# Performance work log

Hardware: AMD Instinct MI355X
Metric: run time of the kernel (lower is better)

## Reference

```python
import jax, jax.numpy as jnp
import numpy as np

NUM_HEADS = 8
NEG_INF = float(-2**32 + 1)
LN_EPS = 1e-8


def setup_inputs() -> dict:
    key = jax.random.key(0)
    ks = jax.random.split(key, 9)
    B, T, D = 4, 2048, 512
    inp = {
        "queries": jax.random.normal(ks[0], (B, T, D), jnp.float32),
        "keys": jax.random.normal(ks[1], (B, T, D), jnp.float32),
        "values": jax.random.normal(ks[2], (B, T, D), jnp.float32),
        "Wq": jax.random.normal(ks[3], (D, D), jnp.float32) / np.sqrt(D),
        "bq": jnp.zeros((D,), jnp.float32),
        "Wk": jax.random.normal(ks[4], (D, D), jnp.float32) / np.sqrt(D),
        "bk": jnp.zeros((D,), jnp.float32),
        "Wv": jax.random.normal(ks[5], (D, D), jnp.float32) / np.sqrt(D),
        "bv": jnp.zeros((D,), jnp.float32),
        "gamma": jnp.ones((D,), jnp.float32),
        "beta": jnp.zeros((D,), jnp.float32),
    }
    return inp


def _split_heads(x, h):
    # torch.cat(torch.chunk(x, h, dim=2), dim=0): [B,T,D] -> [h*B, T, D/h], head-major
    B, T, D = x.shape
    return x.reshape(B, T, h, D // h).transpose(2, 0, 1, 3).reshape(h * B, T, D // h)


def _merge_heads(x, h, B):
    # inverse: [h*B, T, dh] -> [B, T, h*dh]
    hB, T, dh = x.shape
    return x.reshape(h, B, T, dh).transpose(1, 2, 0, 3).reshape(B, T, h * dh)


def reference(queries, keys, values, Wq, bq, Wk, bk, Wv, bv, gamma, beta):
    h = NUM_HEADS
    B, Tq, D = queries.shape
    dh = D // h

    Q = jax.nn.relu(queries @ Wq + bq)
    K = jax.nn.relu(keys @ Wk + bk)
    V = jax.nn.relu(values @ Wv + bv)

    Q_ = _split_heads(Q, h)  # [h*B, Tq, dh]
    K_ = _split_heads(K, h)
    V_ = _split_heads(V, h)

    scores = jnp.einsum('bqd,bkd->bqk', Q_, K_) / jnp.sqrt(jnp.float32(dh))  # [h*B, Tq, Tk]

    # key padding mask: zero rows in `keys` get -inf scores
    key_mask = jnp.sign(jnp.abs(jnp.sum(keys, axis=-1)))  # [B, Tk]
    key_mask = jnp.tile(key_mask, (h, 1))  # [h*B, Tk]
    scores = jnp.where(key_mask[:, None, :] == 0.0, NEG_INF, scores)

    attn = jax.nn.softmax(scores, axis=-1)

    # query mask applied multiplicatively post-softmax
    query_mask = jnp.sign(jnp.abs(jnp.sum(queries, axis=-1)))  # [B, Tq]
    query_mask = jnp.tile(query_mask, (h, 1))  # [h*B, Tq]
    attn = attn * query_mask[:, :, None]

    out = jnp.einsum('bqk,bkd->bqd', attn, V_)  # [h*B, Tq, dh]
    out = _merge_heads(out, h, B) + queries  # residual

    # custom LayerNorm: torch.std is unbiased (ddof=1), eps added to std
    mean = out.mean(-1, keepdims=True)
    std = jnp.sqrt(out.var(-1, ddof=1, keepdims=True))
    return gamma * (out - mean) / (std + LN_EPS) + beta
```

## Files before the change

kernel.cpp:

```cpp
#include <hip/hip_runtime.h>


typedef __attribute__((ext_vector_type(8))) __bf16 bf16x8;
typedef __attribute__((ext_vector_type(4))) float f32x4;

#if __has_builtin(__builtin_amdgcn_exp2f)
#define EXP2F __builtin_amdgcn_exp2f
#else
#define EXP2F exp2f
#endif

#define QSCALE (0.125f * 1.4426950408889634f)

__device__ __forceinline__ unsigned short f2bf(float f) {
  return __builtin_bit_cast(unsigned short, (__bf16)f);
}
__device__ __forceinline__ unsigned pk2(float a, float b) {
  return (unsigned)f2bf(a) | ((unsigned)f2bf(b) << 16);
}
__device__ __forceinline__ f32x4 mfma16(bf16x8 a, bf16x8 b, f32x4 c) {
  return __builtin_amdgcn_mfma_f32_16x16x32_bf16(a, b, c, 0, 0, 0);
}
__device__ __forceinline__ bf16x8 ld_bf8(const unsigned short* p) {
  return *(const bf16x8*)p;
}
__device__ __forceinline__ void g2l16(const void* g, void* l) {
  __builtin_amdgcn_global_load_lds(
      (const __attribute__((address_space(1))) void*)g,
      (__attribute__((address_space(3))) void*)l, 16, 0, 0);
}

__global__ __launch_bounds__(256) void wt_kernel(const float* __restrict__ Wq,
                                                 const float* __restrict__ Wk,
                                                 const float* __restrict__ Wv,
                                                 unsigned short* __restrict__ Wt) {
  int idx = blockIdx.x * 256 + threadIdx.x;
  int o = idx * 8;
  int z = o >> 18;
  int rem = o & 262143;
  int n = rem >> 9;
  int k0 = rem & 511;
  const float* W = (z == 0) ? Wq : ((z == 1) ? Wk : Wv);
  unsigned int w[4];
#pragma unroll
  for (int i = 0; i < 4; ++i) {
    unsigned short lo = f2bf(W[(k0 + 2 * i) * 512 + n]);
    unsigned short hi = f2bf(W[(k0 + 2 * i + 1) * 512 + n]);
    w[i] = (unsigned)lo | ((unsigned)hi << 16);
  }
  *(uint4*)(Wt + o) = make_uint4(w[0], w[1], w[2], w[3]);
}

__global__ __launch_bounds__(256, 3) void proj_kernel(
    const float* __restrict__ Xq, const float* __restrict__ Xk,
    const float* __restrict__ Xv, const float* __restrict__ bq,
    const float* __restrict__ bk, const float* __restrict__ bv,
    const unsigned short* __restrict__ Wt, unsigned short* __restrict__ Qb,
    unsigned short* __restrict__ Kb, unsigned short* __restrict__ Vt,
    float* __restrict__ qmask, float* __restrict__ kmask) {
  __shared__ float Asm[2][128][16];
  __shared__ unsigned short Bsm[128][32];

  int tid = threadIdx.x;
  int m0g = blockIdx.x * 128;
  int z = m0g >> 13;
  int m0 = m0g & 8191;
  int n0 = blockIdx.y * 128;
  const float* X = (z == 0) ? Xq : ((z == 1) ? Xk : Xv);
  const float* bias = (z == 0) ? bq : ((z == 1) ? bk : bv);
  const unsigned short* Wz = Wt + z * 262144;

  int w = tid >> 6, lane = tid & 63;
  int wm = w >> 1, wn = w & 1;
  int mrow = lane & 15, quad = lane >> 4;

  int srow = tid >> 2, schk = tid & 3;
  const float* gA = X + (m0 + srow) * 512 + schk * 4;
  const unsigned short* gB = Wz + (n0 + srow) * 512 + schk * 8;
  char* lA = (char*)&Asm[0][0][0] + tid * 16;
  char* lB = (char*)&Bsm[0][0] + tid * 16;

  const float* rA = &Asm[quad >> 1][0][(quad & 1) * 8];
  const unsigned short* rB = &Bsm[0][quad * 8];

  f32x4 zero = {0.f, 0.f, 0.f, 0.f};
  f32x4 acc[4][4];
#pragma unroll
  for (int i = 0; i < 4; ++i)
#pragma unroll
    for (int j = 0; j < 4; ++j) acc[i][j] = zero;

  bool domask = (z < 2) && (n0 == 0) && (wn == 0);
  float rsum[4] = {0.f, 0.f, 0.f, 0.f};

  for (int kc = 0; kc < 16; ++kc) {
    int ko = kc * 32;
    g2l16(gA + ko, lA);
    g2l16(gA + ko + 64 * 512, lA + 4096);
    g2l16(gA + ko + 16, lA + 8192);
    g2l16(gA + ko + 16 + 64 * 512, lA + 12288);
    g2l16(gB + ko, lB);
    g2l16(gB + ko + 64 * 512, lB + 4096);
    __syncthreads();

    bf16x8 af[4], bfr[4];
#pragma unroll
    for (int mt = 0; mt < 4; ++mt) {
      const float* pa = rA + (wm * 64 + mt * 16 + mrow) * 16;
      f32x4 lo = *(const f32x4*)pa;
      f32x4 hi = *(const f32x4*)(pa + 4);
      if (domask)
        rsum[mt] += lo[0] + lo[1] + lo[2] + lo[3] + hi[0] + hi[1] + hi[2] + hi[3];
      bf16x8 t;
      t[0] = (__bf16)lo[0]; t[1] = (__bf16)lo[1];
      t[2] = (__bf16)lo[2]; t[3] = (__bf16)lo[3];
      t[4] = (__bf16)hi[0]; t[5] = (__bf16)hi[1];
      t[6] = (__bf16)hi[2]; t[7] = (__bf16)hi[3];
      af[mt] = t;
    }
#pragma unroll
    for (int nt = 0; nt < 4; ++nt)
      bfr[nt] = ld_bf8(rB + (wn * 64 + nt * 16 + mrow) * 32);
#pragma unroll
    for (int mt = 0; mt < 4; ++mt)
#pragma unroll
      for (int nt = 0; nt < 4; ++nt)
        acc[mt][nt] = mfma16(af[mt], bfr[nt], acc[mt][nt]);
    __syncthreads();
  }

  if (domask) {
    float* msk = (z == 0) ? qmask : kmask;
#pragma unroll
    for (int mt = 0; mt < 4; ++mt) {
      float s = rsum[mt];
      s += __shfl_xor(s, 16);
      s += __shfl_xor(s, 32);
      if (quad == 0)
        msk[m0 + wm * 64 + mt * 16 + mrow] = (s == 0.f) ? 0.f : 1.f;
    }
  }

  if (z < 2) {
    unsigned short* dst = (z == 0) ? Qb : Kb;
    float sc = (z == 0) ? QSCALE : 1.0f;
#pragma unroll
    for (int nt = 0; nt < 4; ++nt) {
      int n = n0 + wn * 64 + nt * 16 + mrow;
      float bv_ = bias[n];
#pragma unroll
      for (int mt = 0; mt < 4; ++mt) {
        int m = m0 + wm * 64 + mt * 16 + quad * 4;
#pragma unroll
        for (int r = 0; r < 4; ++r) {
          float v = fmaxf(acc[mt][nt][r] + bv_, 0.f) * sc;
          dst[(m + r) * 512 + n] = f2bf(v);
        }
      }
    }
  } else {
#pragma unroll
    for (int nt = 0; nt < 4; ++nt) {
      int n = n0 + wn * 64 + nt * 16 + mrow;
      int hh = n >> 6, jj = n & 63;
      float bv_ = bias[n];
#pragma unroll
      for (int mt = 0; mt < 4; ++mt) {
        int grow = m0 + wm * 64 + mt * 16 + quad * 4;
        int bb = grow >> 11, tl = grow & 2047;
        int pos = (tl & ~31) + quad * 8 + (mt & 1) * 4;
        float p0 = fmaxf(acc[mt][nt][0] + bv_, 0.f);
        float p1 = fmaxf(acc[mt][nt][1] + bv_, 0.f);
        float p2 = fmaxf(acc[mt][nt][2] + bv_, 0.f);
        float p3 = fmaxf(acc[mt][nt][3] + bv_, 0.f);
        *(uint2*)(Vt + ((hh * 4 + bb) * 64 + jj) * 2048 + pos) =
            make_uint2(pk2(p0, p1), pk2(p2, p3));
      }
    }
  }
}

__global__ __launch_bounds__(256, 2) void attn_kernel(
    const unsigned short* __restrict__ Qb, const unsigned short* __restrict__ Kb,
    const unsigned short* __restrict__ Vt, const float* __restrict__ qmask,
    const float* __restrict__ kmask, const float* __restrict__ queries,
    float* __restrict__ out) {
  __shared__ char smem[66560];
  unsigned short* KsmS = (unsigned short*)smem;
  unsigned short* VsmS = (unsigned short*)(smem + 32768);
  float* Obuf = (float*)smem;
  float* lbuf = (float*)(smem + 65536);

  int hb = blockIdx.x;
  int qt = blockIdx.y;
  int h = hb >> 2, b = hb & 3;
  int q0 = qt * 128;
  int tid = threadIdx.x;
  int w = tid >> 6, lane = tid & 63;
  int qh = w >> 1, kh2 = w & 1;
  int mrow = lane & 15, quad = lane >> 4;

  const unsigned short* gK =
      Kb + (b * 2048 + (tid >> 3)) * 512 + h * 64 + (((tid & 7) ^ ((tid >> 3) & 7)) * 8);
  const unsigned short* gV =
      Vt + (hb * 64 + (tid >> 4)) * 2048 + (((tid & 15) ^ ((tid >> 4) & 15)) * 8);

  bf16x8 qf[4][2];
  {
    const unsigned short* qp =
        Qb + (b * 2048 + q0 + qh * 64 + mrow) * 512 + h * 64 + quad * 8;
#pragma unroll
    for (int qn = 0; qn < 4; ++qn) {
      qf[qn][0] = ld_bf8(qp + qn * 8192);
      qf[qn][1] = ld_bf8(qp + qn * 8192 + 32);
    }
  }

  f32x4 zero = {0.f, 0.f, 0.f, 0.f};
  f32x4 oacc[4][4];
#pragma unroll
  for (int i = 0; i < 4; ++i)
#pragma unroll
    for (int j = 0; j < 4; ++j) oacc[i][j] = zero;
  float lpart[4] = {0.f, 0.f, 0.f, 0.f};

  const float* kmB = kmask + b * 2048 + kh2 * 64 + quad * 4;
  const int kfrow = kh2 * 64;
  const int mlow = mrow & 7;

#pragma unroll
  for (int j = 0; j < 4; ++j) {
    g2l16(gK + j * 32 * 512, &KsmS[j * 2048 + tid * 8]);
    g2l16(gV + j * 16 * 2048, &VsmS[j * 2048 + tid * 8]);
  }

  for (int it = 0; it < 16; ++it) {
    int bi = it & 1;
    int kb = it * 128;
    __syncthreads();

    if (it < 15) {
      int nkb = kb + 128;
      int nb = 1 - bi;
#pragma unroll
      for (int j = 0; j < 4; ++j) {
        g2l16(gK + (nkb + j * 32) * 512, &KsmS[nb * 8192 + j * 2048 + tid * 8]);
        g2l16(gV + nkb + j * 16 * 2048, &VsmS[nb * 8192 + j * 2048 + tid * 8]);
      }
    }

    f32x4 kmv[4];
#pragma unroll
    for (int mt = 0; mt < 4; ++mt)
      kmv[mt] = *(const f32x4*)(kmB + kb + mt * 16);

#pragma unroll
    for (int kg = 0; kg < 2; ++kg) {
      bf16x8 kfA0 = ld_bf8(&KsmS[bi * 8192 + (kfrow + kg * 32 + mrow) * 64 +
                                 ((quad) ^ mlow) * 8]);
      bf16x8 kfA1 = ld_bf8(&KsmS[bi * 8192 + (kfrow + kg * 32 + mrow) * 64 +
                                 ((4 + quad) ^ mlow) * 8]);
      bf16x8 kfB0 = ld_bf8(&KsmS[bi * 8192 + (kfrow + kg * 32 + 16 + mrow) * 64 +
                                 ((quad) ^ mlow) * 8]);
      bf16x8 kfB1 = ld_bf8(&KsmS[bi * 8192 + (kfrow + kg * 32 + 16 + mrow) * 64 +
                                 ((4 + quad) ^ mlow) * 8]);
      bf16x8 vfg[4];
#pragma unroll
      for (int dt = 0; dt < 4; ++dt)
        vfg[dt] = ld_bf8(&VsmS[bi * 8192 + (dt * 16 + mrow) * 128 +
                               ((kh2 * 8 + kg * 4 + quad) ^ mrow) * 8]);

      f32x4 sA[4], sB[4];
#pragma unroll
      for (int qn = 0; qn < 4; ++qn) {
        f32x4 s0 = mfma16(kfA0, qf[qn][0], zero);
        sA[qn] = mfma16(kfA1, qf[qn][1], s0);
        f32x4 s1 = mfma16(kfB0, qf[qn][0], zero);
        sB[qn] = mfma16(kfB1, qf[qn][1], s1);
      }
#pragma unroll
      for (int qn = 0; qn < 4; ++qn) {
        f32x4 p0, p1;
#pragma unroll
        for (int r = 0; r < 4; ++r) {
          p0[r] = EXP2F(sA[qn][r]) * kmv[kg * 2][r];
          p1[r] = EXP2F(sB[qn][r]) * kmv[kg * 2 + 1][r];
        }
        lpart[qn] += p0[0] + p0[1] + p0[2] + p0[3] + p1[0] + p1[1] + p1[2] + p1[3];
        bf16x8 pf = __builtin_bit_cast(
            bf16x8, make_uint4(pk2(p0[0], p0[1]), pk2(p0[2], p0[3]),
                               pk2(p1[0], p1[1]), pk2(p1[2], p1[3])));
#pragma unroll
        for (int dt = 0; dt < 4; ++dt)
          oacc[dt][qn] = mfma16(pf, vfg[dt], oacc[dt][qn]);
      }
    }
  }

#pragma unroll
  for (int qn = 0; qn < 4; ++qn) {
    lpart[qn] += __shfl_xor(lpart[qn], 16);
    lpart[qn] += __shfl_xor(lpart[qn], 32);
  }
  __syncthreads();
  if (quad == 0) {
#pragma unroll
    for (int qn = 0; qn < 4; ++qn)
      lbuf[kh2 * 128 + qh * 64 + qn * 16 + mrow] = lpart[qn];
  }
  if (kh2 == 1) {
#pragma unroll
    for (int dt = 0; dt < 4; ++dt)
#pragma unroll
      for (int qn = 0; qn < 4; ++qn)
#pragma unroll
        for (int r = 0; r < 4; ++r)
          Obuf[(qh * 64 + qn * 16 + quad * 4 + r) * 65 + dt * 16 + mrow] =
              oacc[dt][qn][r];
  }
  __syncthreads();
  if (kh2 == 0) {
#pragma unroll
    for (int qn = 0; qn < 4; ++qn) {
#pragma unroll
      for (int r = 0; r < 4; ++r) {
        int qrow = qh * 64 + qn * 16 + quad * 4 + r;
        float l = lbuf[qrow] + lbuf[128 + qrow];
        int qg = b * 2048 + q0 + qrow;
        float inv = qmask[qg] / l;
#pragma unroll
        for (int dt = 0; dt < 4; ++dt) {
          int idx = qg * 512 + h * 64 + dt * 16 + mrow;
          out[idx] =
              (oacc[dt][qn][r] + Obuf[qrow * 65 + dt * 16 + mrow]) * inv +
              queries[idx];
        }
      }
    }
  }
}

__global__ __launch_bounds__(256) void ln_kernel(float* __restrict__ out,
                                                 const float* __restrict__ gamma,
                                                 const float* __restrict__ beta) {
  int row = blockIdx.x * 4 + (threadIdx.x >> 6);
  int lane = threadIdx.x & 63;
  float* p = out + row * 512;
  float4 v1 = ((const float4*)p)[lane];
  float4 v2 = ((const float4*)p)[64 + lane];
  float s = v1.x + v1.y + v1.z + v1.w + v2.x + v2.y + v2.z + v2.w;
  float sq = v1.x * v1.x + v1.y * v1.y + v1.z * v1.z + v1.w * v1.w +
             v2.x * v2.x + v2.y * v2.y + v2.z * v2.z + v2.w * v2.w;
#pragma unroll
  for (int off = 32; off > 0; off >>= 1) {
    s += __shfl_xor(s, off);
    sq += __shfl_xor(sq, off);
  }
  float mean = s * (1.f / 512.f);
  float var = fmaxf((sq - 512.f * mean * mean) * (1.f / 511.f), 0.f);
  float inv = 1.f / (sqrtf(var) + 1e-8f);
  float4 g1 = ((const float4*)gamma)[lane];
  float4 g2 = ((const float4*)gamma)[64 + lane];
  float4 b1 = ((const float4*)beta)[lane];
  float4 b2 = ((const float4*)beta)[64 + lane];
  v1.x = g1.x * (v1.x - mean) * inv + b1.x;
  v1.y = g1.y * (v1.y - mean) * inv + b1.y;
  v1.z = g1.z * (v1.z - mean) * inv + b1.z;
  v1.w = g1.w * (v1.w - mean) * inv + b1.w;
  v2.x = g2.x * (v2.x - mean) * inv + b2.x;
  v2.y = g2.y * (v2.y - mean) * inv + b2.y;
  v2.z = g2.z * (v2.z - mean) * inv + b2.z;
  v2.w = g2.w * (v2.w - mean) * inv + b2.w;
  ((float4*)p)[lane] = v1;
  ((float4*)p)[64 + lane] = v2;
}

extern "C" void kernel_launch(void* const* d_in, const int* in_sizes, int n_in,
                              void* d_out, int out_size, void* d_ws, size_t ws_size,
                              hipStream_t stream) {
  (void)in_sizes; (void)n_in; (void)out_size; (void)ws_size;
  const float* queries = (const float*)d_in[0];
  const float* keys    = (const float*)d_in[1];
  const float* values  = (const float*)d_in[2];
  const float* Wq = (const float*)d_in[3];
  const float* bq = (const float*)d_in[4];
  const float* Wk = (const float*)d_in[5];
  const float* bk = (const float*)d_in[6];
  const float* Wv = (const float*)d_in[7];
  const float* bv = (const float*)d_in[8];
  const float* gamma = (const float*)d_in[9];
  const float* beta  = (const float*)d_in[10];
  float* out = (float*)d_out;

  char* ws = (char*)d_ws;
  unsigned short* Qb = (unsigned short*)(ws);
  unsigned short* Kb = (unsigned short*)(ws + 8 * 1024 * 1024);
  unsigned short* Vt = (unsigned short*)(ws + 16 * 1024 * 1024);
  unsigned short* Wt = (unsigned short*)(ws + 24 * 1024 * 1024);
  float* qmask = (float*)(ws + 24 * 1024 * 1024 + 3 * 512 * 512 * 2);
  float* kmask = qmask + 8192;

  wt_kernel<<<384, 256, 0, stream>>>(Wq, Wk, Wv, Wt);
  proj_kernel<<<dim3(192, 4), 256, 0, stream>>>(queries, keys, values, bq, bk, bv,
                                                Wt, Qb, Kb, Vt, qmask, kmask);
  attn_kernel<<<dim3(32, 16), 256, 0, stream>>>(Qb, Kb, Vt, qmask, kmask, queries, out);
  ln_kernel<<<2048, 256, 0, stream>>>(out, gamma, beta);
}
```

Baseline: 190.5 us.

## Split attention over key halves, fuse combine into LayerNorm, double-buffer projection loads

The attention kernel now splits the key range into two halves across a third grid dimension. Each block handles 128 queries with 4 waves of 32 queries and writes unnormalized partial outputs plus row sums, with the row sums computed by an MFMA against a ones vector. The LayerNorm kernel combines the two partials, applies the query mask, normalization and residual, which removes the in-block shared-memory reduction and raises occupancy and grid size. The projection GEMM also double-buffers its shared-memory tiles, dropping one barrier per step. The cost is extra global traffic for the partial output buffer and row sums.

```diff
diff --git a/kernel.cpp b/kernel.cpp
--- a/kernel.cpp
+++ b/kernel.cpp
@@ -58,8 +58,8 @@
     const unsigned short* __restrict__ Wt, unsigned short* __restrict__ Qb,
     unsigned short* __restrict__ Kb, unsigned short* __restrict__ Vt,
     float* __restrict__ qmask, float* __restrict__ kmask) {
-  __shared__ float Asm[2][128][16];
-  __shared__ unsigned short Bsm[128][32];
+  __shared__ float Asm[2][2][128][16];
+  __shared__ unsigned short Bsm[2][128][32];
 
   int tid = threadIdx.x;
   int m0g = blockIdx.x * 128;
@@ -77,11 +77,6 @@
   int srow = tid >> 2, schk = tid & 3;
   const float* gA = X + (m0 + srow) * 512 + schk * 4;
   const unsigned short* gB = Wz + (n0 + srow) * 512 + schk * 8;
-  char* lA = (char*)&Asm[0][0][0] + tid * 16;
-  char* lB = (char*)&Bsm[0][0] + tid * 16;
-
-  const float* rA = &Asm[quad >> 1][0][(quad & 1) * 8];
-  const unsigned short* rB = &Bsm[0][quad * 8];
 
   f32x4 zero = {0.f, 0.f, 0.f, 0.f};
   f32x4 acc[4][4];
@@ -93,15 +88,35 @@
   bool domask = (z < 2) && (n0 == 0) && (wn == 0);
   float rsum[4] = {0.f, 0.f, 0.f, 0.f};
 
+  {
+    char* lA = (char*)&Asm[0][0][0][0] + tid * 16;
+    char* lB = (char*)&Bsm[0][0][0] + tid * 16;
+    g2l16(gA, lA);
+    g2l16(gA + 64 * 512, lA + 4096);
+    g2l16(gA + 16, lA + 8192);
+    g2l16(gA + 16 + 64 * 512, lA + 12288);
+    g2l16(gB, lB);
+    g2l16(gB + 64 * 512, lB + 4096);
+  }
+
   for (int kc = 0; kc < 16; ++kc) {
-    int ko = kc * 32;
-    g2l16(gA + ko, lA);
-    g2l16(gA + ko + 64 * 512, lA + 4096);
-    g2l16(gA + ko + 16, lA + 8192);
-    g2l16(gA + ko + 16 + 64 * 512, lA + 12288);
-    g2l16(gB + ko, lB);
-    g2l16(gB + ko + 64 * 512, lB + 4096);
+    int bi = kc & 1;
     __syncthreads();
+    if (kc < 15) {
+      int ko = (kc + 1) * 32;
+      int nb = 1 - bi;
+      char* lA = (char*)&Asm[nb][0][0][0] + tid * 16;
+      char* lB = (char*)&Bsm[nb][0][0] + tid * 16;
+      g2l16(gA + ko, lA);
+      g2l16(gA + ko + 64 * 512, lA + 4096);
+      g2l16(gA + ko + 16, lA + 8192);
+      g2l16(gA + ko + 16 + 64 * 512, lA + 12288);
+      g2l16(gB + ko, lB);
+      g2l16(gB + ko + 64 * 512, lB + 4096);
+    }
+
+    const float* rA = &Asm[bi][quad >> 1][0][(quad & 1) * 8];
+    const unsigned short* rB = &Bsm[bi][0][quad * 8];
 
     bf16x8 af[4], bfr[4];
 #pragma unroll
@@ -126,7 +141,6 @@
 #pragma unroll
       for (int nt = 0; nt < 4; ++nt)
         acc[mt][nt] = mfma16(af[mt], bfr[nt], acc[mt][nt]);
-    __syncthreads();
   }
 
   if (domask) {
@@ -180,174 +194,164 @@
   }
 }
 
-__global__ __launch_bounds__(256, 2) void attn_kernel(
+__global__ __launch_bounds__(256, 3) void attn_kernel(
     const unsigned short* __restrict__ Qb, const unsigned short* __restrict__ Kb,
-    const unsigned short* __restrict__ Vt, const float* __restrict__ qmask,
-    const float* __restrict__ kmask, const float* __restrict__ queries,
-    float* __restrict__ out) {
-  __shared__ char smem[66560];
-  unsigned short* KsmS = (unsigned short*)smem;
-  unsigned short* VsmS = (unsigned short*)(smem + 32768);
-  float* Obuf = (float*)smem;
-  float* lbuf = (float*)(smem + 65536);
+    const unsigned short* __restrict__ Vt, const float* __restrict__ kmask,
+    float* __restrict__ Out0, float* __restrict__ Out1,
+    float* __restrict__ lsum) {
+  __shared__ unsigned short Ksm[2][4096];
+  __shared__ unsigned short Vsm[2][4096];
 
   int hb = blockIdx.x;
   int qt = blockIdx.y;
+  int ks = blockIdx.z;
   int h = hb >> 2, b = hb & 3;
   int q0 = qt * 128;
+  int k0 = ks * 1024;
   int tid = threadIdx.x;
   int w = tid >> 6, lane = tid & 63;
-  int qh = w >> 1, kh2 = w & 1;
   int mrow = lane & 15, quad = lane >> 4;
-
-  const unsigned short* gK =
-      Kb + (b * 2048 + (tid >> 3)) * 512 + h * 64 + (((tid & 7) ^ ((tid >> 3) & 7)) * 8);
-  const unsigned short* gV =
-      Vt + (hb * 64 + (tid >> 4)) * 2048 + (((tid & 15) ^ ((tid >> 4) & 15)) * 8);
-
-  bf16x8 qf[4][2];
+  int mlow = mrow & 7;
+
+  int srow = tid >> 3;
+  int sslot = (tid & 7) ^ (srow & 7);
+  const unsigned short* gK = Kb + (b * 2048 + k0 + srow) * 512 + h * 64 + sslot * 8;
+  const unsigned short* gV = Vt + (hb * 64 + srow) * 2048 + k0 + sslot * 8;
+
+  bf16x8 qf[2][2];
   {
     const unsigned short* qp =
-        Qb + (b * 2048 + q0 + qh * 64 + mrow) * 512 + h * 64 + quad * 8;
-#pragma unroll
-    for (int qn = 0; qn < 4; ++qn) {
+        Qb + (b * 2048 + q0 + w * 32 + mrow) * 512 + h * 64 + quad * 8;
+#pragma unroll
+    for (int qn = 0; qn < 2; ++qn) {
       qf[qn][0] = ld_bf8(qp + qn * 8192);
       qf[qn][1] = ld_bf8(qp + qn * 8192 + 32);
     }
   }
 
   f32x4 zero = {0.f, 0.f, 0.f, 0.f};
-  f32x4 oacc[4][4];
-#pragma unroll
-  for (int i = 0; i < 4; ++i)
-#pragma unroll
-    for (int j = 0; j < 4; ++j) oacc[i][j] = zero;
-  float lpart[4] = {0.f, 0.f, 0.f, 0.f};
-
-  const float* kmB = kmask + b * 2048 + kh2 * 64 + quad * 4;
-  const int kfrow = kh2 * 64;
-  const int mlow = mrow & 7;
-
-#pragma unroll
-  for (int j = 0; j < 4; ++j) {
-    g2l16(gK + j * 32 * 512, &KsmS[j * 2048 + tid * 8]);
-    g2l16(gV + j * 16 * 2048, &VsmS[j * 2048 + tid * 8]);
-  }
+  f32x4 oacc[4][2];
+#pragma unroll
+  for (int i = 0; i < 4; ++i) {
+    oacc[i][0] = zero;
+    oacc[i][1] = zero;
+  }
+  f32x4 lacc[2] = {zero, zero};
+  bf16x8 ones;
+#pragma unroll
+  for (int i = 0; i < 8; ++i) ones[i] = (__bf16)1.0f;
+
+  g2l16(gK, &Ksm[0][tid * 8]);
+  g2l16(gK + 32 * 512, &Ksm[0][2048 + tid * 8]);
+  g2l16(gV, &Vsm[0][tid * 8]);
+  g2l16(gV + 32 * 2048, &Vsm[0][2048 + tid * 8]);
 
   for (int it = 0; it < 16; ++it) {
     int bi = it & 1;
-    int kb = it * 128;
     __syncthreads();
-
     if (it < 15) {
-      int nkb = kb + 128;
+      int nof = (it + 1) * 64;
       int nb = 1 - bi;
-#pragma unroll
-      for (int j = 0; j < 4; ++j) {
-        g2l16(gK + (nkb + j * 32) * 512, &KsmS[nb * 8192 + j * 2048 + tid * 8]);
-        g2l16(gV + nkb + j * 16 * 2048, &VsmS[nb * 8192 + j * 2048 + tid * 8]);
-      }
-    }
-
-    f32x4 kmv[4];
-#pragma unroll
-    for (int mt = 0; mt < 4; ++mt)
-      kmv[mt] = *(const f32x4*)(kmB + kb + mt * 16);
+      g2l16(gK + nof * 512, &Ksm[nb][tid * 8]);
+      g2l16(gK + (nof + 32) * 512, &Ksm[nb][2048 + tid * 8]);
+      g2l16(gV + nof, &Vsm[nb][tid * 8]);
+      g2l16(gV + nof + 32 * 2048, &Vsm[nb][2048 + tid * 8]);
+    }
+
+    const float* kmc = kmask + b * 2048 + k0 + it * 64 + quad * 4;
+    f32x4 km00 = *(const f32x4*)(kmc);
+    f32x4 km01 = *(const f32x4*)(kmc + 16);
+    f32x4 km10 = *(const f32x4*)(kmc + 32);
+    f32x4 km11 = *(const f32x4*)(kmc + 48);
 
 #pragma unroll
     for (int kg = 0; kg < 2; ++kg) {
-      bf16x8 kfA0 = ld_bf8(&KsmS[bi * 8192 + (kfrow + kg * 32 + mrow) * 64 +
-                                 ((quad) ^ mlow) * 8]);
-      bf16x8 kfA1 = ld_bf8(&KsmS[bi * 8192 + (kfrow + kg * 32 + mrow) * 64 +
-                                 ((4 + quad) ^ mlow) * 8]);
-      bf16x8 kfB0 = ld_bf8(&KsmS[bi * 8192 + (kfrow + kg * 32 + 16 + mrow) * 64 +
-                                 ((quad) ^ mlow) * 8]);
-      bf16x8 kfB1 = ld_bf8(&KsmS[bi * 8192 + (kfrow + kg * 32 + 16 + mrow) * 64 +
-                                 ((4 + quad) ^ mlow) * 8]);
-      bf16x8 vfg[4];
+      bf16x8 kf00 = ld_bf8(&Ksm[bi][(kg * 32 + mrow) * 64 + ((quad) ^ mlow) * 8]);
+      bf16x8 kf01 = ld_bf8(&Ksm[bi][(kg * 32 + mrow) * 64 + ((4 + quad) ^ mlow) * 8]);
+      bf16x8 kf10 = ld_bf8(&Ksm[bi][(kg * 32 + 16 + mrow) * 64 + ((quad) ^ mlow) * 8]);
+      bf16x8 kf11 = ld_bf8(&Ksm[bi][(kg * 32 + 16 + mrow) * 64 + ((4 + quad) ^ mlow) * 8]);
+      bf16x8 vf[4];
 #pragma unroll
       for (int dt = 0; dt < 4; ++dt)
-        vfg[dt] = ld_bf8(&VsmS[bi * 8192 + (dt * 16 + mrow) * 128 +
-                               ((kh2 * 8 + kg * 4 + quad) ^ mrow) * 8]);
-
-      f32x4 sA[4], sB[4];
-#pragma unroll
-      for (int qn = 0; qn < 4; ++qn) {
-        f32x4 s0 = mfma16(kfA0, qf[qn][0], zero);
-        sA[qn] = mfma16(kfA1, qf[qn][1], s0);
-        f32x4 s1 = mfma16(kfB0, qf[qn][0], zero);
-        sB[qn] = mfma16(kfB1, qf[qn][1], s1);
-      }
-#pragma unroll
-      for (int qn = 0; qn < 4; ++qn) {
+        vf[dt] = ld_bf8(&Vsm[bi][(dt * 16 + mrow) * 64 + ((kg * 4 + quad) ^ mlow) * 8]);
+      f32x4 kma = kg ? km10 : km00;
+      f32x4 kmb = kg ? km11 : km01;
+
+#pragma unroll
+      for (int qn = 0; qn < 2; ++qn) {
+        f32x4 s0 = mfma16(kf00, qf[qn][0], zero);
+        s0 = mfma16(kf01, qf[qn][1], s0);
+        f32x4 s1 = mfma16(kf10, qf[qn][0], zero);
+        s1 = mfma16(kf11, qf[qn][1], s1);
         f32x4 p0, p1;
 #pragma unroll
         for (int r = 0; r < 4; ++r) {
-          p0[r] = EXP2F(sA[qn][r]) * kmv[kg * 2][r];
-          p1[r] = EXP2F(sB[qn][r]) * kmv[kg * 2 + 1][r];
+          p0[r] = EXP2F(s0[r]) * kma[r];
+          p1[r] = EXP2F(s1[r]) * kmb[r];
         }
-        lpart[qn] += p0[0] + p0[1] + p0[2] + p0[3] + p1[0] + p1[1] + p1[2] + p1[3];
         bf16x8 pf = __builtin_bit_cast(
             bf16x8, make_uint4(pk2(p0[0], p0[1]), pk2(p0[2], p0[3]),
                                pk2(p1[0], p1[1]), pk2(p1[2], p1[3])));
+        lacc[qn] = mfma16(pf, ones, lacc[qn]);
 #pragma unroll
         for (int dt = 0; dt < 4; ++dt)
-          oacc[dt][qn] = mfma16(pf, vfg[dt], oacc[dt][qn]);
+          oacc[dt][qn] = mfma16(pf, vf[dt], oacc[dt][qn]);
       }
     }
   }
 
-#pragma unroll
-  for (int qn = 0; qn < 4; ++qn) {
-    lpart[qn] += __shfl_xor(lpart[qn], 16);
-    lpart[qn] += __shfl_xor(lpart[qn], 32);
-  }
-  __syncthreads();
-  if (quad == 0) {
-#pragma unroll
-    for (int qn = 0; qn < 4; ++qn)
-      lbuf[kh2 * 128 + qh * 64 + qn * 16 + mrow] = lpart[qn];
-  }
-  if (kh2 == 1) {
-#pragma unroll
-    for (int dt = 0; dt < 4; ++dt)
-#pragma unroll
-      for (int qn = 0; qn < 4; ++qn)
-#pragma unroll
-        for (int r = 0; r < 4; ++r)
-          Obuf[(qh * 64 + qn * 16 + quad * 4 + r) * 65 + dt * 16 + mrow] =
-              oacc[dt][qn][r];
-  }
-  __syncthreads();
-  if (kh2 == 0) {
-#pragma unroll
-    for (int qn = 0; qn < 4; ++qn) {
-#pragma unroll
-      for (int r = 0; r < 4; ++r) {
-        int qrow = qh * 64 + qn * 16 + quad * 4 + r;
-        float l = lbuf[qrow] + lbuf[128 + qrow];
-        int qg = b * 2048 + q0 + qrow;
-        float inv = qmask[qg] / l;
-#pragma unroll
-        for (int dt = 0; dt < 4; ++dt) {
-          int idx = qg * 512 + h * 64 + dt * 16 + mrow;
-          out[idx] =
-              (oacc[dt][qn][r] + Obuf[qrow * 65 + dt * 16 + mrow]) * inv +
-              queries[idx];
-        }
-      }
-    }
-  }
-}
-
-__global__ __launch_bounds__(256) void ln_kernel(float* __restrict__ out,
-                                                 const float* __restrict__ gamma,
-                                                 const float* __restrict__ beta) {
+  float* Op = ks ? Out1 : Out0;
+#pragma unroll
+  for (int qn = 0; qn < 2; ++qn) {
+#pragma unroll
+    for (int r = 0; r < 4; ++r) {
+      int qg = b * 2048 + q0 + w * 32 + qn * 16 + quad * 4 + r;
+#pragma unroll
+      for (int dt = 0; dt < 4; ++dt)
+        Op[qg * 512 + h * 64 + dt * 16 + mrow] = oacc[dt][qn][r];
+    }
+    if (mrow == 0) {
+#pragma unroll
+      for (int r = 0; r < 4; ++r)
+        lsum[ks * 65536 + hb * 2048 + q0 + w * 32 + qn * 16 + quad * 4 + r] =
+            lacc[qn][r];
+    }
+  }
+}
+
+__global__ __launch_bounds__(256) void ln_kernel(
+    float* __restrict__ out, const float* __restrict__ O1,
+    const float* __restrict__ lsum, const float* __restrict__ qmask,
+    const float* __restrict__ queries, const float* __restrict__ gamma,
+    const float* __restrict__ beta) {
   int row = blockIdx.x * 4 + (threadIdx.x >> 6);
   int lane = threadIdx.x & 63;
-  float* p = out + row * 512;
-  float4 v1 = ((const float4*)p)[lane];
-  float4 v2 = ((const float4*)p)[64 + lane];
+  int b = row >> 11, t = row & 2047;
+  int h0 = lane >> 4, h1 = 4 + (lane >> 4);
+
+  float qm = qmask[row];
+  float la = lsum[(h0 * 4 + b) * 2048 + t] + lsum[65536 + (h0 * 4 + b) * 2048 + t];
+  float lb_ = lsum[(h1 * 4 + b) * 2048 + t] + lsum[65536 + (h1 * 4 + b) * 2048 + t];
+  float inva = qm / la, invb = qm / lb_;
+
+  const float* p = out + row * 512;
+  float4 o1 = ((const float4*)p)[lane];
+  float4 o2 = ((const float4*)p)[64 + lane];
+  float4 w1 = ((const float4*)(O1 + row * 512))[lane];
+  float4 w2 = ((const float4*)(O1 + row * 512))[64 + lane];
+  float4 q1 = ((const float4*)(queries + row * 512))[lane];
+  float4 q2 = ((const float4*)(queries + row * 512))[64 + lane];
+
+  float4 v1, v2;
+  v1.x = (o1.x + w1.x) * inva + q1.x;
+  v1.y = (o1.y + w1.y) * inva + q1.y;
+  v1.z = (o1.z + w1.z) * inva + q1.z;
+  v1.w = (o1.w + w1.w) * inva + q1.w;
+  v2.x = (o2.x + w2.x) * invb + q2.x;
+  v2.y = (o2.y + w2.y) * invb + q2.y;
+  v2.z = (o2.z + w2.z) * invb + q2.z;
+  v2.w = (o2.w + w2.w) * invb + q2.w;
+
   float s = v1.x + v1.y + v1.z + v1.w + v2.x + v2.y + v2.z + v2.w;
   float sq = v1.x * v1.x + v1.y * v1.y + v1.z * v1.z + v1.w * v1.w +
              v2.x * v2.x + v2.y * v2.y + v2.z * v2.z + v2.w * v2.w;
@@ -359,6 +363,7 @@
   float mean = s * (1.f / 512.f);
   float var = fmaxf((sq - 512.f * mean * mean) * (1.f / 511.f), 0.f);
   float inv = 1.f / (sqrtf(var) + 1e-8f);
+
   float4 g1 = ((const float4*)gamma)[lane];
   float4 g2 = ((const float4*)gamma)[64 + lane];
   float4 b1 = ((const float4*)beta)[lane];
@@ -371,8 +376,9 @@
   v2.y = g2.y * (v2.y - mean) * inv + b2.y;
   v2.z = g2.z * (v2.z - mean) * inv + b2.z;
   v2.w = g2.w * (v2.w - mean) * inv + b2.w;
-  ((float4*)p)[lane] = v1;
-  ((float4*)p)[64 + lane] = v2;
+  float* pw = out + row * 512;
+  ((float4*)pw)[lane] = v1;
+  ((float4*)pw)[64 + lane] = v2;
 }
 
 extern "C" void kernel_launch(void* const* d_in, const int* in_sizes, int n_in,
@@ -399,10 +405,12 @@
   unsigned short* Wt = (unsigned short*)(ws + 24 * 1024 * 1024);
   float* qmask = (float*)(ws + 24 * 1024 * 1024 + 3 * 512 * 512 * 2);
   float* kmask = qmask + 8192;
+  float* O1   = (float*)(ws + 26 * 1024 * 1024);
+  float* lsum = (float*)(ws + 26 * 1024 * 1024 + 4 * 2048 * 512 * 4);
 
   wt_kernel<<<384, 256, 0, stream>>>(Wq, Wk, Wv, Wt);
   proj_kernel<<<dim3(192, 4), 256, 0, stream>>>(queries, keys, values, bq, bk, bv,
                                                 Wt, Qb, Kb, Vt, qmask, kmask);
-  attn_kernel<<<dim3(32, 16), 256, 0, stream>>>(Qb, Kb, Vt, qmask, kmask, queries, out);
-  ln_kernel<<<2048, 256, 0, stream>>>(out, gamma, beta);
-}
+  attn_kernel<<<dim3(32, 16, 2), 256, 0, stream>>>(Qb, Kb, Vt, kmask, out, O1, lsum);
+  ln_kernel<<<2048, 256, 0, stream>>>(out, O1, lsum, qmask, queries, gamma, beta);
+}
```

Result: slower. 197.1 us (+3.5%).
